# Kernel tuning notes

Hardware: AMD Instinct MI355X
Metric: run time of the kernel (lower is better)

Reference implementation:

```python
import jax, jax.numpy as jnp
import numpy as np

NUM_HEADS = 16


def setup_inputs() -> dict:
    key = jax.random.key(0)
    ks = jax.random.split(key, 4)
    B, N, C = 4, 1024, 1024
    H, D = NUM_HEADS, C // NUM_HEADS
    L_cache = 4096
    x = jax.random.normal(ks[0], (B, N, C), dtype=jnp.float32)
    kv_cache = jax.random.normal(ks[1], (2, B, H, L_cache, D), dtype=jnp.float32)
    w_qkv = jax.random.normal(ks[2], (C, 3 * C), dtype=jnp.float32) * (C ** -0.5)
    w_proj = jax.random.normal(ks[3], (C, C), dtype=jnp.float32) * (C ** -0.5)
    b_proj = jnp.zeros((C,), dtype=jnp.float32)
    return {"x": x, "kv_cache": kv_cache, "w_qkv": w_qkv, "w_proj": w_proj, "b_proj": b_proj}


def reference(x, kv_cache, w_qkv, w_proj, b_proj):
    B, N, C = x.shape
    H = NUM_HEADS
    D = C // H
    scale = D ** -0.5
    # QKV projection (no bias), split into q,k,v with shape [B,H,N,D]
    qkv = (x @ w_qkv).reshape(B, N, 3, H, D).transpose(2, 0, 3, 1, 4)
    q, k, v = qkv[0], qkv[1], qkv[2]
    # concat KV cache along sequence axis -> [B,H,L_cache+N,D]
    k = jnp.concatenate([kv_cache[0], k], axis=2)
    v = jnp.concatenate([kv_cache[1], v], axis=2)
    # scaled dot-product attention (no causal mask, eval mode: no dropout)
    attn = jax.nn.softmax(jnp.einsum('bhnd,bhld->bhnl', q * scale, k), axis=-1)
    out = jnp.einsum('bhnl,bhld->bhnd', attn, v)  # [B,H,N,D]
    out = out.transpose(0, 2, 1, 3).reshape(B, N, C)
    return out @ w_proj + b_proj
```

## Files before the change

kernel.cpp:

```cpp
#include <hip/hip_runtime.h>

typedef short  s16x8 __attribute__((ext_vector_type(8)));
typedef float  f32x4 __attribute__((ext_vector_type(4)));

#define B_   4
#define N_   1024
#define C_   1024
#define H_   16
#define D_   64
#define LC_  4096
#define LT_  5120
#define KVHALF_ 16777216

#define SM_C1 0.18033688011f

static __device__ __forceinline__ unsigned short f2bf(float x) {
    union { float f; unsigned int u; } c; c.f = x;
    unsigned int r = (c.u + 0x7FFFu + ((c.u >> 16) & 1u)) >> 16;
    return (unsigned short)r;
}
static __device__ __forceinline__ float exp2fast(float x) {
#if __has_builtin(__builtin_amdgcn_exp2f)
    return __builtin_amdgcn_exp2f(x);
#else
    return exp2f(x);
#endif
}
static __device__ __forceinline__ unsigned int pk2(float lo, float hi) {
    union { float f; unsigned int u; } cl, ch;
    cl.f = lo; ch.f = hi;
    return __builtin_amdgcn_perm(ch.u + 0x8000u, cl.u + 0x8000u, 0x07060302u);
}
static __device__ __forceinline__ s16x8 cvt8f(const float* p) {
    f32x4 a = *(const f32x4*)p;
    f32x4 b = *(const f32x4*)(p + 4);
    s16x8 r;
#pragma unroll
    for (int j = 0; j < 4; ++j) {
        r[j]     = (short)f2bf(a[j]);
        r[j + 4] = (short)f2bf(b[j]);
    }
    return r;
}
static __device__ __forceinline__ f32x4 mfma16(s16x8 a, s16x8 b, f32x4 c) {
    return __builtin_amdgcn_mfma_f32_16x16x32_bf16(a, b, c, 0, 0, 0);
}

static __device__ __forceinline__ int vt_addr(int d, int k) {
    return d * 72 + ((((k >> 3) ^ ((d >> 3) & 7)) & 7) << 3) + (k & 7);
}
static __device__ __forceinline__ int bt_addr(int n, int k) {
    return n * 40 + ((((k >> 3) ^ (n >> 3)) & 3) << 3) + (k & 7);
}

__global__ __launch_bounds__(256) void convert_bf(const float* __restrict__ src,
                                                  unsigned short* __restrict__ dst,
                                                  int total8)
{
    size_t stride = (size_t)gridDim.x * blockDim.x;
    for (size_t i = blockIdx.x * blockDim.x + threadIdx.x; i < (size_t)total8; i += stride)
        *(s16x8*)(dst + i * 8) = cvt8f(src + i * 8);
}

__global__ __launch_bounds__(256) void transpose_v(const float* __restrict__ vsrc,
                                                   unsigned short* __restrict__ vdst)
{
    __shared__ __attribute__((aligned(16))) unsigned short tlds[64 * 72];
    const int tid = threadIdx.x;
    const int bh = blockIdx.x >> 6;
    const int l0 = (blockIdx.x & 63) * 64;
    {
        const int lrow = tid >> 2, d0 = (tid & 3) * 16;
        const float* p = vsrc + ((size_t)bh * LC_ + l0 + lrow) * D_ + d0;
        s16x8 a = cvt8f(p), b = cvt8f(p + 8);
#pragma unroll
        for (int j = 0; j < 8; ++j) {
            tlds[vt_addr(d0 + j, lrow)]     = (unsigned short)a[j];
            tlds[vt_addr(d0 + 8 + j, lrow)] = (unsigned short)b[j];
        }
    }
    __syncthreads();
    {
        const int d = tid >> 2, lo = (tid & 3) * 16;
        const int kb = lo >> 3, sd = (d >> 3) & 7;
        s16x8 v0 = *(const s16x8*)&tlds[d * 72 + ((kb ^ sd) << 3)];
        s16x8 v1 = *(const s16x8*)&tlds[d * 72 + (((kb + 1) ^ sd) << 3)];
        unsigned short* q = vdst + ((size_t)bh * D_ + d) * LC_ + l0 + lo;
        *(s16x8*)q = v0;
        *(s16x8*)(q + 8) = v1;
    }
}

template <int NN, int KK>
__global__ __launch_bounds__(256) void transpose_w(const float* __restrict__ src,
                                                   unsigned short* __restrict__ dst)
{
    __shared__ __attribute__((aligned(16))) unsigned short tlds[64 * 72];
    const int tid = threadIdx.x;
    const int n0 = blockIdx.x * 64;
    const int k0 = blockIdx.y * 64;
    {
        const int kl = tid >> 2, c0 = (tid & 3) * 16;
        const float* p = src + (size_t)(k0 + kl) * NN + n0 + c0;
        s16x8 a = cvt8f(p), b = cvt8f(p + 8);
#pragma unroll
        for (int j = 0; j < 8; ++j) {
            tlds[vt_addr(c0 + j, kl)]     = (unsigned short)a[j];
            tlds[vt_addr(c0 + 8 + j, kl)] = (unsigned short)b[j];
        }
    }
    __syncthreads();
    {
        const int nl = tid >> 2, ko = (tid & 3) * 16;
        const int kb = ko >> 3, sd = (nl >> 3) & 7;
        s16x8 v0 = *(const s16x8*)&tlds[nl * 72 + ((kb ^ sd) << 3)];
        s16x8 v1 = *(const s16x8*)&tlds[nl * 72 + (((kb + 1) ^ sd) << 3)];
        unsigned short* q = dst + (size_t)(n0 + nl) * KK + k0 + ko;
        *(s16x8*)q = v0;
        *(s16x8*)(q + 8) = v1;
    }
}

template <int NW, int MODE>
__global__ __launch_bounds__(256) void gemm128(
    const unsigned short* __restrict__ A,
    const unsigned short* __restrict__ BwT,
    const float* __restrict__ bias,
    unsigned short* __restrict__ out0,
    unsigned short* __restrict__ out1,
    unsigned short* __restrict__ out2,
    float* __restrict__ outf,
    int K)
{
    __shared__ __attribute__((aligned(16))) unsigned short Alds[128 * 40];
    __shared__ __attribute__((aligned(16))) unsigned short BT[128 * 40];

    const int tid = threadIdx.x;
    const int w  = tid >> 6;
    const int l  = tid & 63;
    const int g  = l >> 4;
    const int li = l & 15;
    const int wr = w >> 1;
    const int wc = w & 1;
    const int bm = blockIdx.y * 128;
    const int bn = blockIdx.x * 128;

    f32x4 acc[4][4] = {};

    const int srow = tid >> 1;
    const int sko  = (tid & 1) * 16;

    for (int k0 = 0; k0 < K; k0 += 32) {
        {
            const unsigned short* p = A + (size_t)(bm + srow) * K + k0 + sko;
            *(s16x8*)&Alds[srow * 40 + sko]     = *(const s16x8*)p;
            *(s16x8*)&Alds[srow * 40 + sko + 8] = *(const s16x8*)(p + 8);
        }
        {
            const unsigned short* p = BwT + (size_t)(bn + srow) * K + k0 + sko;
            *(s16x8*)&BT[bt_addr(srow, sko)]     = *(const s16x8*)p;
            *(s16x8*)&BT[bt_addr(srow, sko + 8)] = *(const s16x8*)(p + 8);
        }
        __syncthreads();

        s16x8 ar[4], br[4];
#pragma unroll
        for (int i = 0; i < 4; ++i)
            ar[i] = *(const s16x8*)&Alds[(wr * 64 + i * 16 + li) * 40 + g * 8];
#pragma unroll
        for (int j = 0; j < 4; ++j)
            br[j] = *(const s16x8*)&BT[bt_addr(wc * 64 + j * 16 + li, g * 8)];
#pragma unroll
        for (int i = 0; i < 4; ++i)
#pragma unroll
            for (int j = 0; j < 4; ++j)
                acc[i][j] = mfma16(ar[i], br[j], acc[i][j]);
        __syncthreads();
    }

    if (MODE == 0) {
        const int which = bn >> 10;
        const int b     = bm >> 10;
#pragma unroll
        for (int j = 0; j < 4; ++j) {
            const int c = (bn & 1023) + wc * 64 + j * 16 + li;
            const int h = c >> 6;
            const int d = c & 63;
#pragma unroll
            for (int i = 0; i < 4; ++i) {
#pragma unroll
                for (int r = 0; r < 4; ++r) {
                    const int m = bm + wr * 64 + i * 16 + g * 4 + r;
                    const int n = m & 1023;
                    if (which == 0)
                        out0[((size_t)((b * H_ + h) * N_ + n)) * D_ + d] =
                            f2bf(acc[i][j][r] * SM_C1);
                    else if (which == 1)
                        out1[((size_t)((b * H_ + h) * N_ + n)) * D_ + d] =
                            f2bf(acc[i][j][r]);
                    else
                        out2[((size_t)((b * H_ + h) * D_ + d)) * N_ + n] =
                            f2bf(acc[i][j][r]);
                }
            }
        }
    } else {
#pragma unroll
        for (int j = 0; j < 4; ++j) {
            const int c = bn + wc * 64 + j * 16 + li;
            const float bv = bias[c];
#pragma unroll
            for (int i = 0; i < 4; ++i) {
#pragma unroll
                for (int r = 0; r < 4; ++r) {
                    const int m = bm + wr * 64 + i * 16 + g * 4 + r;
                    outf[(size_t)m * NW + c] = acc[i][j][r] + bv;
                }
            }
        }
    }
}

__global__ __launch_bounds__(256) void attn_single(
    const unsigned short* __restrict__ qbuf,
    const unsigned short* __restrict__ knew,
    const unsigned short* __restrict__ vnewT,
    const unsigned short* __restrict__ kcbf,
    const unsigned short* __restrict__ vtcbf,
    unsigned short* __restrict__ x2)
{
    __shared__ __attribute__((aligned(16))) unsigned short Klds[64 * 72];
    __shared__ __attribute__((aligned(16))) unsigned short VT[64 * 72];

    const int tid  = threadIdx.x;
    const int w    = tid >> 6;
    const int l    = tid & 63;
    const int g    = l >> 4;
    const int li   = l & 15;

    const int i0   = blockIdx.x;
    const int xcd  = i0 & 7;
    const int j0   = i0 >> 3;
    const int bh   = xcd * 8 + (j0 >> 4);
    const int qblk = j0 & 15;

    s16x8 ones;
    {
        const short ov = (li == 0) ? (short)0x3F80 : (short)0;
#pragma unroll
        for (int j = 0; j < 8; ++j) ones[j] = ov;
    }

    const unsigned short* qrowp =
        qbuf + ((size_t)bh * N_ + qblk * 64 + w * 16 + li) * D_;
    const s16x8 qf0 = *(const s16x8*)(qrowp + g * 8);
    const s16x8 qf1 = *(const s16x8*)(qrowp + 32 + g * 8);

    f32x4 acc[5] = {};

    const int kr = tid >> 2;
    const int ko = (tid & 3) * 16;
    s16x8 kreg0, kreg1, vreg0, vreg1;

    auto LOAD = [&](int t) {
        const int key0 = t * 64;
        if (t < LC_ / 64) {
            const unsigned short* ks = kcbf + ((size_t)bh * LC_ + key0 + kr) * D_ + ko;
            kreg0 = *(const s16x8*)ks; kreg1 = *(const s16x8*)(ks + 8);
            const unsigned short* vs = vtcbf + ((size_t)bh * D_ + kr) * LC_ + key0 + ko;
            vreg0 = *(const s16x8*)vs; vreg1 = *(const s16x8*)(vs + 8);
        } else {
            const unsigned short* ks = knew + ((size_t)bh * N_ + (key0 - LC_) + kr) * D_ + ko;
            kreg0 = *(const s16x8*)ks; kreg1 = *(const s16x8*)(ks + 8);
            const unsigned short* vs = vnewT + ((size_t)bh * D_ + kr) * N_ + (key0 - LC_) + ko;
            vreg0 = *(const s16x8*)vs; vreg1 = *(const s16x8*)(vs + 8);
        }
    };
    LOAD(0);

    const int kb  = ko >> 3;
    const int sdw = (kr >> 3) & 7;

    for (int t = 0; t < LT_ / 64; ++t) {
        __syncthreads();
        *(s16x8*)&Klds[kr * 72 + ko]     = kreg0;
        *(s16x8*)&Klds[kr * 72 + ko + 8] = kreg1;
        *(s16x8*)&VT[kr * 72 + ((kb ^ sdw) << 3)]       = vreg0;
        *(s16x8*)&VT[kr * 72 + (((kb + 1) ^ sdw) << 3)] = vreg1;
        if (t + 1 < LT_ / 64) LOAD(t + 1);
        __syncthreads();

        f32x4 sc[4];
#pragma unroll
        for (int ct = 0; ct < 4; ++ct) {
            f32x4 s = {};
            s16x8 ka0 = *(const s16x8*)&Klds[(ct * 16 + li) * 72 + g * 8];
            s16x8 ka1 = *(const s16x8*)&Klds[(ct * 16 + li) * 72 + 32 + g * 8];
            s = mfma16(ka0, qf0, s);
            sc[ct] = mfma16(ka1, qf1, s);
        }

        unsigned int pk[4][2];
#pragma unroll
        for (int ct = 0; ct < 4; ++ct) {
            float p0 = exp2fast(sc[ct][0]);
            float p1 = exp2fast(sc[ct][1]);
            float p2 = exp2fast(sc[ct][2]);
            float p3 = exp2fast(sc[ct][3]);
            pk[ct][0] = pk2(p0, p1);
            pk[ct][1] = pk2(p2, p3);
        }

        unsigned int a0 = pk[0][0], b0 = pk[1][0];
        asm("v_permlane32_swap_b32 %0, %1" : "+v"(a0), "+v"(b0));
        asm("v_permlane16_swap_b32 %0, %1" : "+v"(a0), "+v"(b0));
        unsigned int a1 = pk[0][1], b1 = pk[1][1];
        asm("v_permlane32_swap_b32 %0, %1" : "+v"(a1), "+v"(b1));
        asm("v_permlane16_swap_b32 %0, %1" : "+v"(a1), "+v"(b1));
        unsigned int c0 = pk[2][0], e0 = pk[3][0];
        asm("v_permlane32_swap_b32 %0, %1" : "+v"(c0), "+v"(e0));
        asm("v_permlane16_swap_b32 %0, %1" : "+v"(c0), "+v"(e0));
        unsigned int c1 = pk[2][1], e1 = pk[3][1];
        asm("v_permlane32_swap_b32 %0, %1" : "+v"(c1), "+v"(e1));
        asm("v_permlane16_swap_b32 %0, %1" : "+v"(c1), "+v"(e1));

        union { unsigned int u[4]; s16x8 v; } P0, P1;
        P0.u[0] = a0; P0.u[1] = a1; P0.u[2] = b0; P0.u[3] = b1;
        P1.u[0] = c0; P1.u[1] = c1; P1.u[2] = e0; P1.u[3] = e1;
        const s16x8 pf0 = P0.v, pf1 = P1.v;

#pragma unroll
        for (int dt = 0; dt < 4; ++dt) {
            const int vrow = dt * 16 + li;
            const int sd = (vrow >> 3) & 7;
            s16x8 vb0 = *(const s16x8*)&VT[vrow * 72 + ((g ^ sd) << 3)];
            s16x8 vb1 = *(const s16x8*)&VT[vrow * 72 + (((4 + g) ^ sd) << 3)];
            acc[dt] = mfma16(pf0, vb0, acc[dt]);
            acc[dt] = mfma16(pf1, vb1, acc[dt]);
        }
        acc[4] = mfma16(pf0, ones, acc[4]);
        acc[4] = mfma16(pf1, ones, acc[4]);
    }

    float linv[4];
#pragma unroll
    for (int r = 0; r < 4; ++r)
        linv[r] = 1.0f / __shfl(acc[4][r], l & 48);
    const int b = bh >> 4, h = bh & 15;
#pragma unroll
    for (int dt = 0; dt < 4; ++dt) {
#pragma unroll
        for (int r = 0; r < 4; ++r) {
            int qrow = qblk * 64 + w * 16 + g * 4 + r;
            x2[((size_t)(b * N_ + qrow)) * C_ + h * D_ + dt * 16 + li] =
                f2bf(acc[dt][r] * linv[r]);
        }
    }
}

extern "C" void kernel_launch(void* const* d_in, const int* in_sizes, int n_in,
                              void* d_out, int out_size, void* d_ws, size_t ws_size,
                              hipStream_t stream)
{
    const float* x      = (const float*)d_in[0];
    const float* kv     = (const float*)d_in[1];
    const float* w_qkv  = (const float*)d_in[2];
    const float* w_proj = (const float*)d_in[3];
    const float* b_proj = (const float*)d_in[4];
    float* out = (float*)d_out;

    unsigned short* kcbf  = (unsigned short*)d_ws;
    unsigned short* vtcbf = kcbf + KVHALF_;
    unsigned short* q     = vtcbf + KVHALF_;
    unsigned short* knew  = q + 4194304;
    unsigned short* vnewT = knew + 4194304;
    unsigned short* tail  = vnewT + 4194304;

    unsigned short* xbf = tail;
    unsigned short* x2  = tail;
    unsigned short* wqT = tail + 4194304;
    unsigned short* wpT = tail + 4194304;

    convert_bf<<<dim3(2048), 256, 0, stream>>>(x, xbf, 524288);
    transpose_w<3072, 1024><<<dim3(48, 16), 256, 0, stream>>>(w_qkv, wqT);
    convert_bf<<<dim3(2048), 256, 0, stream>>>(kv, kcbf, KVHALF_ / 8);
    transpose_v<<<dim3(64 * 64), 256, 0, stream>>>(kv + KVHALF_, vtcbf);

    gemm128<3072, 0><<<dim3(24, 32), 256, 0, stream>>>(
        xbf, wqT, nullptr, q, knew, vnewT, nullptr, C_);

    attn_single<<<dim3(B_ * H_ * (N_ / 64)), 256, 0, stream>>>(
        q, knew, vnewT, kcbf, vtcbf, x2);

    transpose_w<1024, 1024><<<dim3(16, 16), 256, 0, stream>>>(w_proj, wpT);
    gemm128<1024, 1><<<dim3(8, 32), 256, 0, stream>>>(
        x2, wpT, b_proj, nullptr, nullptr, nullptr, out, C_);
}
```

Measured before the change: 262.7 us.

## Fuse conversion prepasses into one kernel and double-buffer attention K/V tiles

Merges the separate bf16 conversion and transpose launches (x, KV cache, V transpose, both weight transposes) into a single prepass kernel that picks its job by block-index range, and moves the w_proj buffer so it no longer aliases wqT. The attention loop now keeps two LDS buffers for K and V, writing the next tile while computing on the current one with a single barrier per iteration. The aim is to cut launch overhead and tail gaps between the small kernels, and to remove one sync per attention step. The cost is doubled attention LDS use, which can lower occupancy.

After: 254.4 us. 1.03x faster.

```diff
diff --git a/kernel.cpp b/kernel.cpp
--- a/kernel.cpp
+++ b/kernel.cpp
@@ -10,6 +10,7 @@
 #define D_   64
 #define LC_  4096
 #define LT_  5120
+#define NT_  80
 #define KVHALF_ 16777216
 
 #define SM_C1 0.18033688011f
@@ -53,71 +54,69 @@
     return n * 40 + ((((k >> 3) ^ (n >> 3)) & 3) << 3) + (k & 7);
 }
 
-__global__ __launch_bounds__(256) void convert_bf(const float* __restrict__ src,
-                                                  unsigned short* __restrict__ dst,
-                                                  int total8)
+static __device__ void tr_tile(const float* __restrict__ src, int sstride,
+                               unsigned short* __restrict__ dst, int dstride,
+                               int tid, unsigned short* tlds)
 {
-    size_t stride = (size_t)gridDim.x * blockDim.x;
-    for (size_t i = blockIdx.x * blockDim.x + threadIdx.x; i < (size_t)total8; i += stride)
-        *(s16x8*)(dst + i * 8) = cvt8f(src + i * 8);
-}
-
-__global__ __launch_bounds__(256) void transpose_v(const float* __restrict__ vsrc,
-                                                   unsigned short* __restrict__ vdst)
+    {
+        const int r = tid >> 2, c0 = (tid & 3) * 16;
+        const float* p = src + (size_t)r * sstride + c0;
+        s16x8 a = cvt8f(p), b = cvt8f(p + 8);
+#pragma unroll
+        for (int j = 0; j < 8; ++j) {
+            tlds[vt_addr(c0 + j, r)]     = (unsigned short)a[j];
+            tlds[vt_addr(c0 + 8 + j, r)] = (unsigned short)b[j];
+        }
+    }
+    __syncthreads();
+    {
+        const int c = tid >> 2, ro = (tid & 3) * 16;
+        const int kb = ro >> 3, sd = (c >> 3) & 7;
+        s16x8 v0 = *(const s16x8*)&tlds[c * 72 + ((kb ^ sd) << 3)];
+        s16x8 v1 = *(const s16x8*)&tlds[c * 72 + (((kb + 1) ^ sd) << 3)];
+        unsigned short* q = dst + (size_t)c * dstride + ro;
+        *(s16x8*)q = v0;
+        *(s16x8*)(q + 8) = v1;
+    }
+}
+
+__global__ __launch_bounds__(256) void prepass(
+    const float* __restrict__ x, const float* __restrict__ kv,
+    const float* __restrict__ w_qkv, const float* __restrict__ w_proj,
+    unsigned short* __restrict__ xbf, unsigned short* __restrict__ kcbf,
+    unsigned short* __restrict__ vtcbf, unsigned short* __restrict__ wqT,
+    unsigned short* __restrict__ wpT)
 {
     __shared__ __attribute__((aligned(16))) unsigned short tlds[64 * 72];
     const int tid = threadIdx.x;
-    const int bh = blockIdx.x >> 6;
-    const int l0 = (blockIdx.x & 63) * 64;
-    {
-        const int lrow = tid >> 2, d0 = (tid & 3) * 16;
-        const float* p = vsrc + ((size_t)bh * LC_ + l0 + lrow) * D_ + d0;
-        s16x8 a = cvt8f(p), b = cvt8f(p + 8);
-#pragma unroll
-        for (int j = 0; j < 8; ++j) {
-            tlds[vt_addr(d0 + j, lrow)]     = (unsigned short)a[j];
-            tlds[vt_addr(d0 + 8 + j, lrow)] = (unsigned short)b[j];
-        }
-    }
-    __syncthreads();
-    {
-        const int d = tid >> 2, lo = (tid & 3) * 16;
-        const int kb = lo >> 3, sd = (d >> 3) & 7;
-        s16x8 v0 = *(const s16x8*)&tlds[d * 72 + ((kb ^ sd) << 3)];
-        s16x8 v1 = *(const s16x8*)&tlds[d * 72 + (((kb + 1) ^ sd) << 3)];
-        unsigned short* q = vdst + ((size_t)bh * D_ + d) * LC_ + l0 + lo;
-        *(s16x8*)q = v0;
-        *(s16x8*)(q + 8) = v1;
-    }
-}
-
-template <int NN, int KK>
-__global__ __launch_bounds__(256) void transpose_w(const float* __restrict__ src,
-                                                   unsigned short* __restrict__ dst)
-{
-    __shared__ __attribute__((aligned(16))) unsigned short tlds[64 * 72];
-    const int tid = threadIdx.x;
-    const int n0 = blockIdx.x * 64;
-    const int k0 = blockIdx.y * 64;
-    {
-        const int kl = tid >> 2, c0 = (tid & 3) * 16;
-        const float* p = src + (size_t)(k0 + kl) * NN + n0 + c0;
-        s16x8 a = cvt8f(p), b = cvt8f(p + 8);
-#pragma unroll
-        for (int j = 0; j < 8; ++j) {
-            tlds[vt_addr(c0 + j, kl)]     = (unsigned short)a[j];
-            tlds[vt_addr(c0 + 8 + j, kl)] = (unsigned short)b[j];
-        }
-    }
-    __syncthreads();
-    {
-        const int nl = tid >> 2, ko = (tid & 3) * 16;
-        const int kb = ko >> 3, sd = (nl >> 3) & 7;
-        s16x8 v0 = *(const s16x8*)&tlds[nl * 72 + ((kb ^ sd) << 3)];
-        s16x8 v1 = *(const s16x8*)&tlds[nl * 72 + (((kb + 1) ^ sd) << 3)];
-        unsigned short* q = dst + (size_t)(n0 + nl) * KK + k0 + ko;
-        *(s16x8*)q = v0;
-        *(s16x8*)(q + 8) = v1;
+    const int bid = blockIdx.x;
+
+    if (bid < 2048) {
+        const size_t total8 = (size_t)KVHALF_ / 8;
+        const size_t stride = (size_t)2048 * 256;
+        for (size_t i = (size_t)bid * 256 + tid; i < total8; i += stride)
+            *(s16x8*)(kcbf + i * 8) = cvt8f(kv + i * 8);
+    } else if (bid < 6144) {
+        const int ti = bid - 2048;
+        const int bh = ti >> 6;
+        const int l0 = (ti & 63) * 64;
+        tr_tile(kv + KVHALF_ + ((size_t)bh * LC_ + l0) * D_, D_,
+                vtcbf + (size_t)bh * D_ * LC_ + l0, LC_, tid, tlds);
+    } else if (bid < 6912) {
+        const int ti = bid - 6144;
+        const int n0 = (ti % 48) * 64;
+        const int k0 = (ti / 48) * 64;
+        tr_tile(w_qkv + (size_t)k0 * 3072 + n0, 3072,
+                wqT + (size_t)n0 * 1024 + k0, 1024, tid, tlds);
+    } else if (bid < 7168) {
+        const int ti = bid - 6912;
+        const int n0 = (ti & 15) * 64;
+        const int k0 = (ti >> 4) * 64;
+        tr_tile(w_proj + (size_t)k0 * 1024 + n0, 1024,
+                wpT + (size_t)n0 * 1024 + k0, 1024, tid, tlds);
+    } else {
+        const size_t i = (size_t)(bid - 7168) * 256 + tid;
+        *(s16x8*)(xbf + i * 8) = cvt8f(x + i * 8);
     }
 }
 
@@ -229,8 +228,8 @@
     const unsigned short* __restrict__ vtcbf,
     unsigned short* __restrict__ x2)
 {
-    __shared__ __attribute__((aligned(16))) unsigned short Klds[64 * 72];
-    __shared__ __attribute__((aligned(16))) unsigned short VT[64 * 72];
+    __shared__ __attribute__((aligned(16))) unsigned short Klds[2][64 * 72];
+    __shared__ __attribute__((aligned(16))) unsigned short VT[2][64 * 72];
 
     const int tid  = threadIdx.x;
     const int w    = tid >> 6;
@@ -276,26 +275,34 @@
             vreg0 = *(const s16x8*)vs; vreg1 = *(const s16x8*)(vs + 8);
         }
     };
-    LOAD(0);
 
     const int kb  = ko >> 3;
     const int sdw = (kr >> 3) & 7;
 
-    for (int t = 0; t < LT_ / 64; ++t) {
-        __syncthreads();
-        *(s16x8*)&Klds[kr * 72 + ko]     = kreg0;
-        *(s16x8*)&Klds[kr * 72 + ko + 8] = kreg1;
-        *(s16x8*)&VT[kr * 72 + ((kb ^ sdw) << 3)]       = vreg0;
-        *(s16x8*)&VT[kr * 72 + (((kb + 1) ^ sdw) << 3)] = vreg1;
-        if (t + 1 < LT_ / 64) LOAD(t + 1);
-        __syncthreads();
+    LOAD(0);
+    *(s16x8*)&Klds[0][kr * 72 + ko]     = kreg0;
+    *(s16x8*)&Klds[0][kr * 72 + ko + 8] = kreg1;
+    *(s16x8*)&VT[0][kr * 72 + ((kb ^ sdw) << 3)]       = vreg0;
+    *(s16x8*)&VT[0][kr * 72 + (((kb + 1) ^ sdw) << 3)] = vreg1;
+    LOAD(1);
+    __syncthreads();
+
+    for (int t = 0; t < NT_; ++t) {
+        const int cur = t & 1, nxt = cur ^ 1;
+        if (t + 1 < NT_) {
+            *(s16x8*)&Klds[nxt][kr * 72 + ko]     = kreg0;
+            *(s16x8*)&Klds[nxt][kr * 72 + ko + 8] = kreg1;
+            *(s16x8*)&VT[nxt][kr * 72 + ((kb ^ sdw) << 3)]       = vreg0;
+            *(s16x8*)&VT[nxt][kr * 72 + (((kb + 1) ^ sdw) << 3)] = vreg1;
+        }
+        if (t + 2 < NT_) LOAD(t + 2);
 
         f32x4 sc[4];
 #pragma unroll
         for (int ct = 0; ct < 4; ++ct) {
             f32x4 s = {};
-            s16x8 ka0 = *(const s16x8*)&Klds[(ct * 16 + li) * 72 + g * 8];
-            s16x8 ka1 = *(const s16x8*)&Klds[(ct * 16 + li) * 72 + 32 + g * 8];
+            s16x8 ka0 = *(const s16x8*)&Klds[cur][(ct * 16 + li) * 72 + g * 8];
+            s16x8 ka1 = *(const s16x8*)&Klds[cur][(ct * 16 + li) * 72 + 32 + g * 8];
             s = mfma16(ka0, qf0, s);
             sc[ct] = mfma16(ka1, qf1, s);
         }
@@ -333,13 +340,15 @@
         for (int dt = 0; dt < 4; ++dt) {
             const int vrow = dt * 16 + li;
             const int sd = (vrow >> 3) & 7;
-            s16x8 vb0 = *(const s16x8*)&VT[vrow * 72 + ((g ^ sd) << 3)];
-            s16x8 vb1 = *(const s16x8*)&VT[vrow * 72 + (((4 + g) ^ sd) << 3)];
+            s16x8 vb0 = *(const s16x8*)&VT[cur][vrow * 72 + ((g ^ sd) << 3)];
+            s16x8 vb1 = *(const s16x8*)&VT[cur][vrow * 72 + (((4 + g) ^ sd) << 3)];
             acc[dt] = mfma16(pf0, vb0, acc[dt]);
             acc[dt] = mfma16(pf1, vb1, acc[dt]);
         }
         acc[4] = mfma16(pf0, ones, acc[4]);
         acc[4] = mfma16(pf1, ones, acc[4]);
+
+        __syncthreads();
     }
 
     float linv[4];
@@ -379,12 +388,10 @@
     unsigned short* xbf = tail;
     unsigned short* x2  = tail;
     unsigned short* wqT = tail + 4194304;
-    unsigned short* wpT = tail + 4194304;
-
-    convert_bf<<<dim3(2048), 256, 0, stream>>>(x, xbf, 524288);
-    transpose_w<3072, 1024><<<dim3(48, 16), 256, 0, stream>>>(w_qkv, wqT);
-    convert_bf<<<dim3(2048), 256, 0, stream>>>(kv, kcbf, KVHALF_ / 8);
-    transpose_v<<<dim3(64 * 64), 256, 0, stream>>>(kv + KVHALF_, vtcbf);
+    unsigned short* wpT = tail + 7340032;
+
+    prepass<<<dim3(9216), 256, 0, stream>>>(
+        x, kv, w_qkv, w_proj, xbf, kcbf, vtcbf, wqT, wpT);
 
     gemm128<3072, 0><<<dim3(24, 32), 256, 0, stream>>>(
         xbf, wqT, nullptr, q, knew, vnewT, nullptr, C_);
@@ -392,7 +399,6 @@
     attn_single<<<dim3(B_ * H_ * (N_ / 64)), 256, 0, stream>>>(
         q, knew, vnewT, kcbf, vtcbf, x2);
 
-    transpose_w<1024, 1024><<<dim3(16, 16), 256, 0, stream>>>(w_proj, wpT);
     gemm128<1024, 1><<<dim3(8, 32), 256, 0, stream>>>(
         x2, wpT, b_proj, nullptr, nullptr, nullptr, out, C_);
 }
```
